# Performance work log

Measured on AMD Instinct MI355X. Metric: run time of the kernel, lower is better.

Reference implementation:

```python
import jax, jax.numpy as jnp
import numpy as np

N_NODES = 50000
N_EDGES = 800000
D_IN = 64
D_HID = 64
D_OUT = 64


def setup_inputs() -> dict:
    key = jax.random.key(0)
    ks = jax.random.split(key, 9)
    x = jax.random.normal(ks[0], (N_NODES, D_IN), dtype=jnp.float32)
    src = jax.random.randint(ks[1], (N_EDGES,), 0, N_NODES, dtype=jnp.int64)
    dst = jax.random.randint(ks[2], (N_EDGES,), 0, N_NODES, dtype=jnp.int64)
    s0 = 1.0 / np.sqrt(D_IN)
    s1 = 1.0 / np.sqrt(D_HID)
    W_self0 = jax.random.normal(ks[3], (D_IN, D_HID), dtype=jnp.float32) * s0
    W_neigh0 = jax.random.normal(ks[4], (D_IN, D_HID), dtype=jnp.float32) * s0
    b0 = jnp.zeros((D_HID,), dtype=jnp.float32)
    W_self1 = jax.random.normal(ks[5], (D_HID, D_OUT), dtype=jnp.float32) * s1
    W_neigh1 = jax.random.normal(ks[6], (D_HID, D_OUT), dtype=jnp.float32) * s1
    b1 = jnp.zeros((D_OUT,), dtype=jnp.float32)
    return {"x": x, "src": src, "dst": dst,
            "W_self0": W_self0, "W_neigh0": W_neigh0, "b0": b0,
            "W_self1": W_self1, "W_neigh1": W_neigh1, "b1": b1}


def reference(x, src, dst, W_self0, W_neigh0, b0, W_self1, W_neigh1, b1):
    n = x.shape[0]
    # in-degree per destination node; clamp to 1 for isolated nodes (DGL behavior)
    deg = jax.ops.segment_sum(jnp.ones(src.shape[0], dtype=x.dtype), dst, num_segments=n)
    inv_deg = (1.0 / jnp.maximum(deg, 1.0))[:, None]  # [N,1]

    def sage_mean(h, W_self, W_neigh, b):
        # gather src features, mean-reduce onto dst, then linear combine
        agg = jax.ops.segment_sum(h[src], dst, num_segments=n)  # [N,d]
        neigh = agg * inv_deg
        return h @ W_self + neigh @ W_neigh + b

    # layer 0: SAGEConv with internal relu activation
    h = jax.nn.relu(sage_mean(x, W_self0, W_neigh0, b0))
    # outer relu in GraphSAGE_Full.forward (idempotent after internal relu)
    h = jax.nn.relu(h)
    # dropout rate 0.0 -> identity
    # final layer: no activation
    h = sage_mean(h, W_self1, W_neigh1, b1)
    return h
```

## Files before the change

### kernel.cpp

```cpp
#include <hip/hip_runtime.h>

#define N_NODES 50000
#define N_EDGES 800000
#define D 64
#define NSLICE 8
#define SLICE_N ((N_NODES + NSLICE - 1) / NSLICE)
#define BCAP 64

__device__ __forceinline__ unsigned short f2bf(float f) {
    unsigned int u = __builtin_bit_cast(unsigned int, f);
    u += 0x7fffu + ((u >> 16) & 1u);
    return (unsigned short)(u >> 16);
}
__device__ __forceinline__ float bflo(unsigned int u) {
    return __builtin_bit_cast(float, u << 16);
}
__device__ __forceinline__ float bfhi(unsigned int u) {
    return __builtin_bit_cast(float, u & 0xffff0000u);
}

__global__ __launch_bounds__(256) void k_fill2(const int* __restrict__ src,
                                               const int* __restrict__ dst,
                                               int* __restrict__ cnt,
                                               int* __restrict__ csr) {
    int slice = blockIdx.x & (NSLICE - 1);
    int lo = slice * SLICE_N, hi = lo + SLICE_N;
    int gblk = blockIdx.x >> 3, nblk = gridDim.x >> 3;
    for (int e = gblk * blockDim.x + threadIdx.x; e < N_EDGES; e += nblk * blockDim.x) {
        int d = dst[e];
        if (d >= lo && d < hi) {
            int p = atomicAdd(&cnt[d], 1);
            csr[(d << 6) + p] = src[e];
        }
    }
}

__global__ __launch_bounds__(256, 4) void k_xform(const float* __restrict__ h,
        const float* __restrict__ Ws, const float* __restrict__ Wn,
        const float* __restrict__ b,
        float* __restrict__ yS, unsigned short* __restrict__ yN) {
    int lane = threadIdx.x & 63;
    int gwave = __builtin_amdgcn_readfirstlane((blockIdx.x * blockDim.x + threadIdx.x) >> 6);
    int nwaves = (gridDim.x * blockDim.x) >> 6;

    int mat = gwave & 1;
    const float* W = mat ? Wn : Ws;

    float w[D];
#pragma unroll
    for (int k = 0; k < D; ++k) w[k] = W[k * D + lane];
    float bj = mat ? 0.f : b[lane];

    const int ngroups = (N_NODES + 3) / 4;
    for (int g = gwave >> 1; g < ngroups; g += (nwaves >> 1)) {
        const float* x0 = h + (size_t)(g * 4) * D;
        float a0 = bj, a1 = bj, a2 = bj, a3 = bj;
#pragma unroll
        for (int kq = 0; kq < 16; ++kq) {
            float4 v0 = *(const float4*)(x0 + 0 * D + kq * 4);
            float4 v1 = *(const float4*)(x0 + 1 * D + kq * 4);
            float4 v2 = *(const float4*)(x0 + 2 * D + kq * 4);
            float4 v3 = *(const float4*)(x0 + 3 * D + kq * 4);
            a0 = fmaf(v0.x, w[kq * 4 + 0], a0);
            a1 = fmaf(v1.x, w[kq * 4 + 0], a1);
            a2 = fmaf(v2.x, w[kq * 4 + 0], a2);
            a3 = fmaf(v3.x, w[kq * 4 + 0], a3);
            a0 = fmaf(v0.y, w[kq * 4 + 1], a0);
            a1 = fmaf(v1.y, w[kq * 4 + 1], a1);
            a2 = fmaf(v2.y, w[kq * 4 + 1], a2);
            a3 = fmaf(v3.y, w[kq * 4 + 1], a3);
            a0 = fmaf(v0.z, w[kq * 4 + 2], a0);
            a1 = fmaf(v1.z, w[kq * 4 + 2], a1);
            a2 = fmaf(v2.z, w[kq * 4 + 2], a2);
            a3 = fmaf(v3.z, w[kq * 4 + 2], a3);
            a0 = fmaf(v0.w, w[kq * 4 + 3], a0);
            a1 = fmaf(v1.w, w[kq * 4 + 3], a1);
            a2 = fmaf(v2.w, w[kq * 4 + 3], a2);
            a3 = fmaf(v3.w, w[kq * 4 + 3], a3);
        }
        size_t base = (size_t)(g * 4) * D + lane;
        if (mat) {
            yN[base + 0 * D] = f2bf(a0);
            yN[base + 1 * D] = f2bf(a1);
            yN[base + 2 * D] = f2bf(a2);
            yN[base + 3 * D] = f2bf(a3);
        } else {
            yS[base + 0 * D] = a0;
            yS[base + 1 * D] = a1;
            yS[base + 2 * D] = a2;
            yS[base + 3 * D] = a3;
        }
    }
}

__global__ __launch_bounds__(256) void k_aggf(const char* __restrict__ yN,
        const float* __restrict__ yS,
        const int* __restrict__ cnt, const int* __restrict__ csr,
        float* __restrict__ out, int relu) {
    int node = __builtin_amdgcn_readfirstlane((blockIdx.x * blockDim.x + threadIdx.x) >> 6);
    int lane = threadIdx.x & 63;
    if (node >= N_NODES) return;
    int q = lane >> 4;
    int fq = lane & 15;
    int deg = cnt[node];
    const int* bucket = csr + (node << 6);
    unsigned foff = (unsigned)fq * 8u;

    float s0 = 0.f, s1 = 0.f, s2 = 0.f, s3 = 0.f;

#define ROUND16(E0)                                                         \
    {                                                                       \
        int i0 = (E0) + q, i1 = i0 + 4, i2 = i0 + 8, i3 = i0 + 12;          \
        int b0 = bucket[i0], b1 = bucket[i1], b2 = bucket[i2], b3 = bucket[i3]; \
        unsigned a0 = (i0 < deg) ? ((unsigned)b0 << 7) : 0u;                \
        unsigned a1 = (i1 < deg) ? ((unsigned)b1 << 7) : 0u;                \
        unsigned a2 = (i2 < deg) ? ((unsigned)b2 << 7) : 0u;                \
        unsigned a3 = (i3 < deg) ? ((unsigned)b3 << 7) : 0u;                \
        float m0 = (i0 < deg) ? 1.f : 0.f;                                  \
        float m1 = (i1 < deg) ? 1.f : 0.f;                                  \
        float m2 = (i2 < deg) ? 1.f : 0.f;                                  \
        float m3 = (i3 < deg) ? 1.f : 0.f;                                  \
        uint2 u0 = *(const uint2*)(yN + a0 + foff);                         \
        uint2 u1 = *(const uint2*)(yN + a1 + foff);                         \
        uint2 u2 = *(const uint2*)(yN + a2 + foff);                         \
        uint2 u3 = *(const uint2*)(yN + a3 + foff);                         \
        s0 = fmaf(m0, bflo(u0.x), s0); s0 = fmaf(m1, bflo(u1.x), s0);       \
        s0 = fmaf(m2, bflo(u2.x), s0); s0 = fmaf(m3, bflo(u3.x), s0);       \
        s1 = fmaf(m0, bfhi(u0.x), s1); s1 = fmaf(m1, bfhi(u1.x), s1);       \
        s1 = fmaf(m2, bfhi(u2.x), s1); s1 = fmaf(m3, bfhi(u3.x), s1);       \
        s2 = fmaf(m0, bflo(u0.y), s2); s2 = fmaf(m1, bflo(u1.y), s2);       \
        s2 = fmaf(m2, bflo(u2.y), s2); s2 = fmaf(m3, bflo(u3.y), s2);       \
        s3 = fmaf(m0, bfhi(u0.y), s3); s3 = fmaf(m1, bfhi(u1.y), s3);       \
        s3 = fmaf(m2, bfhi(u2.y), s3); s3 = fmaf(m3, bfhi(u3.y), s3);       \
    }

    ROUND16(0)
    if (deg > 16) ROUND16(16)
    if (deg > 32) {
        ROUND16(32)
        if (deg > 48) ROUND16(48)
    }
#undef ROUND16

    s0 += __shfl_xor(s0, 16, 64);  s0 += __shfl_xor(s0, 32, 64);
    s1 += __shfl_xor(s1, 16, 64);  s1 += __shfl_xor(s1, 32, 64);
    s2 += __shfl_xor(s2, 16, 64);  s2 += __shfl_xor(s2, 32, 64);
    s3 += __shfl_xor(s3, 16, 64);  s3 += __shfl_xor(s3, 32, 64);

    float sv = (q == 0) ? s0 : (q == 1) ? s1 : (q == 2) ? s2 : s3;
    int f = fq * 4 + q;
    float self = yS[(size_t)node * D + f];
    float inv = 1.0f / fmaxf((float)deg, 1.0f);
    float acc = self + sv * inv;
    if (relu) acc = fmaxf(acc, 0.f);
    out[(size_t)node * D + f] = acc;
}

extern "C" void kernel_launch(void* const* d_in, const int* in_sizes, int n_in,
                              void* d_out, int out_size, void* d_ws, size_t ws_size,
                              hipStream_t stream) {
    const float* x   = (const float*)d_in[0];
    const int*   src = (const int*)d_in[1];
    const int*   dst = (const int*)d_in[2];
    const float* Ws0 = (const float*)d_in[3];
    const float* Wn0 = (const float*)d_in[4];
    const float* b0  = (const float*)d_in[5];
    const float* Ws1 = (const float*)d_in[6];
    const float* Wn1 = (const float*)d_in[7];
    const float* b1  = (const float*)d_in[8];
    float* out = (float*)d_out;

    char* p = (char*)d_ws;
    float*          yS  = (float*)p;          p += (size_t)N_NODES * D * sizeof(float);
    unsigned short* yN  = (unsigned short*)p; p += (size_t)N_NODES * D * sizeof(unsigned short);
    int* cnt = (int*)p;                       p += (size_t)N_NODES * sizeof(int);
    int* csr = (int*)p;                       p += (size_t)N_NODES * BCAP * sizeof(int);

    hipMemsetAsync(cnt, 0, (size_t)N_NODES * sizeof(int), stream);

    k_fill2<<<1024, 256, 0, stream>>>(src, dst, cnt, csr);

    const int aggBlocks = (N_NODES + 3) / 4;

    k_xform<<<1024, 256, 0, stream>>>(x, Ws0, Wn0, b0, yS, yN);
    k_aggf<<<aggBlocks, 256, 0, stream>>>((const char*)yN, yS, cnt, csr, out, 1);

    k_xform<<<1024, 256, 0, stream>>>(out, Ws1, Wn1, b1, yS, yN);
    k_aggf<<<aggBlocks, 256, 0, stream>>>((const char*)yN, yS, cnt, csr, out, 0);
}
```

Before: 198.8 us.

## Split bf16 neighbor features into two half-width planes mapped to XCD halves

The transform kernel now writes the bf16 neighbor projection as two separate 32-feature arrays instead of one interleaved 64-feature array. The aggregation kernel assigns blocks so that XCDs 0-3 gather from one half-plane and XCDs 4-7 from the other. Each XCD's L2 should then only need to cache a 3.2 MB half-table rather than the full table, improving gather hit rates. Each node is now processed by two waves, each reading 64-byte rows, which doubles the bucket index reads and leaves half the lanes idle at writeback.

```diff
diff --git a/kernel.cpp b/kernel.cpp
--- a/kernel.cpp
+++ b/kernel.cpp
@@ -38,7 +38,8 @@
 __global__ __launch_bounds__(256, 4) void k_xform(const float* __restrict__ h,
         const float* __restrict__ Ws, const float* __restrict__ Wn,
         const float* __restrict__ b,
-        float* __restrict__ yS, unsigned short* __restrict__ yN) {
+        float* __restrict__ yS,
+        unsigned short* __restrict__ yNa, unsigned short* __restrict__ yNb) {
     int lane = threadIdx.x & 63;
     int gwave = __builtin_amdgcn_readfirstlane((blockIdx.x * blockDim.x + threadIdx.x) >> 6);
     int nwaves = (gridDim.x * blockDim.x) >> 6;
@@ -50,6 +51,9 @@
 #pragma unroll
     for (int k = 0; k < D; ++k) w[k] = W[k * D + lane];
     float bj = mat ? 0.f : b[lane];
+
+    unsigned short* yH = (lane < 32) ? yNa : yNb;
+    int fl = lane & 31;
 
     const int ngroups = (N_NODES + 3) / 4;
     for (int g = gwave >> 1; g < ngroups; g += (nwaves >> 1)) {
@@ -78,13 +82,14 @@
             a2 = fmaf(v2.w, w[kq * 4 + 3], a2);
             a3 = fmaf(v3.w, w[kq * 4 + 3], a3);
         }
-        size_t base = (size_t)(g * 4) * D + lane;
+        int row = g * 4;
         if (mat) {
-            yN[base + 0 * D] = f2bf(a0);
-            yN[base + 1 * D] = f2bf(a1);
-            yN[base + 2 * D] = f2bf(a2);
-            yN[base + 3 * D] = f2bf(a3);
+            yH[(row + 0) * 32 + fl] = f2bf(a0);
+            yH[(row + 1) * 32 + fl] = f2bf(a1);
+            yH[(row + 2) * 32 + fl] = f2bf(a2);
+            yH[(row + 3) * 32 + fl] = f2bf(a3);
         } else {
+            size_t base = (size_t)row * D + lane;
             yS[base + 0 * D] = a0;
             yS[base + 1 * D] = a1;
             yS[base + 2 * D] = a2;
@@ -93,37 +98,42 @@
     }
 }
 
-__global__ __launch_bounds__(256) void k_aggf(const char* __restrict__ yN,
+__global__ __launch_bounds__(256) void k_aggf2(const char* __restrict__ yA,
+        const char* __restrict__ yB,
         const float* __restrict__ yS,
         const int* __restrict__ cnt, const int* __restrict__ csr,
         float* __restrict__ out, int relu) {
-    int node = __builtin_amdgcn_readfirstlane((blockIdx.x * blockDim.x + threadIdx.x) >> 6);
+    int xcd  = blockIdx.x & 7;
+    int half = xcd >> 2;
+    int g    = (blockIdx.x >> 3) * 4 + (xcd & 3);
+    int node = __builtin_amdgcn_readfirstlane((g << 2) + (int)(threadIdx.x >> 6));
+    const char* yH = half ? yB : yA;
+    int ho = half << 5;
     int lane = threadIdx.x & 63;
-    if (node >= N_NODES) return;
-    int q = lane >> 4;
-    int fq = lane & 15;
+    int q  = lane >> 3;
+    int fq = lane & 7;
     int deg = cnt[node];
     const int* bucket = csr + (node << 6);
     unsigned foff = (unsigned)fq * 8u;
 
     float s0 = 0.f, s1 = 0.f, s2 = 0.f, s3 = 0.f;
 
-#define ROUND16(E0)                                                         \
+#define ROUND32(E0)                                                         \
     {                                                                       \
-        int i0 = (E0) + q, i1 = i0 + 4, i2 = i0 + 8, i3 = i0 + 12;          \
+        int i0 = (E0) + q, i1 = i0 + 8, i2 = i0 + 16, i3 = i0 + 24;         \
         int b0 = bucket[i0], b1 = bucket[i1], b2 = bucket[i2], b3 = bucket[i3]; \
-        unsigned a0 = (i0 < deg) ? ((unsigned)b0 << 7) : 0u;                \
-        unsigned a1 = (i1 < deg) ? ((unsigned)b1 << 7) : 0u;                \
-        unsigned a2 = (i2 < deg) ? ((unsigned)b2 << 7) : 0u;                \
-        unsigned a3 = (i3 < deg) ? ((unsigned)b3 << 7) : 0u;                \
+        unsigned a0 = (i0 < deg) ? ((unsigned)b0 << 6) : 0u;                \
+        unsigned a1 = (i1 < deg) ? ((unsigned)b1 << 6) : 0u;                \
+        unsigned a2 = (i2 < deg) ? ((unsigned)b2 << 6) : 0u;                \
+        unsigned a3 = (i3 < deg) ? ((unsigned)b3 << 6) : 0u;                \
         float m0 = (i0 < deg) ? 1.f : 0.f;                                  \
         float m1 = (i1 < deg) ? 1.f : 0.f;                                  \
         float m2 = (i2 < deg) ? 1.f : 0.f;                                  \
         float m3 = (i3 < deg) ? 1.f : 0.f;                                  \
-        uint2 u0 = *(const uint2*)(yN + a0 + foff);                         \
-        uint2 u1 = *(const uint2*)(yN + a1 + foff);                         \
-        uint2 u2 = *(const uint2*)(yN + a2 + foff);                         \
-        uint2 u3 = *(const uint2*)(yN + a3 + foff);                         \
+        uint2 u0 = *(const uint2*)(yH + a0 + foff);                         \
+        uint2 u1 = *(const uint2*)(yH + a1 + foff);                         \
+        uint2 u2 = *(const uint2*)(yH + a2 + foff);                         \
+        uint2 u3 = *(const uint2*)(yH + a3 + foff);                         \
         s0 = fmaf(m0, bflo(u0.x), s0); s0 = fmaf(m1, bflo(u1.x), s0);       \
         s0 = fmaf(m2, bflo(u2.x), s0); s0 = fmaf(m3, bflo(u3.x), s0);       \
         s1 = fmaf(m0, bfhi(u0.x), s1); s1 = fmaf(m1, bfhi(u1.x), s1);       \
@@ -134,26 +144,24 @@
         s3 = fmaf(m2, bfhi(u2.y), s3); s3 = fmaf(m3, bfhi(u3.y), s3);       \
     }
 
-    ROUND16(0)
-    if (deg > 16) ROUND16(16)
-    if (deg > 32) {
-        ROUND16(32)
-        if (deg > 48) ROUND16(48)
-    }
-#undef ROUND16
-
-    s0 += __shfl_xor(s0, 16, 64);  s0 += __shfl_xor(s0, 32, 64);
-    s1 += __shfl_xor(s1, 16, 64);  s1 += __shfl_xor(s1, 32, 64);
-    s2 += __shfl_xor(s2, 16, 64);  s2 += __shfl_xor(s2, 32, 64);
-    s3 += __shfl_xor(s3, 16, 64);  s3 += __shfl_xor(s3, 32, 64);
-
-    float sv = (q == 0) ? s0 : (q == 1) ? s1 : (q == 2) ? s2 : s3;
-    int f = fq * 4 + q;
-    float self = yS[(size_t)node * D + f];
-    float inv = 1.0f / fmaxf((float)deg, 1.0f);
-    float acc = self + sv * inv;
-    if (relu) acc = fmaxf(acc, 0.f);
-    out[(size_t)node * D + f] = acc;
+    ROUND32(0)
+    if (deg > 32) ROUND32(32)
+#undef ROUND32
+
+    s0 += __shfl_xor(s0, 8, 64); s0 += __shfl_xor(s0, 16, 64); s0 += __shfl_xor(s0, 32, 64);
+    s1 += __shfl_xor(s1, 8, 64); s1 += __shfl_xor(s1, 16, 64); s1 += __shfl_xor(s1, 32, 64);
+    s2 += __shfl_xor(s2, 8, 64); s2 += __shfl_xor(s2, 16, 64); s2 += __shfl_xor(s2, 32, 64);
+    s3 += __shfl_xor(s3, 8, 64); s3 += __shfl_xor(s3, 16, 64); s3 += __shfl_xor(s3, 32, 64);
+
+    if (q < 4) {
+        int f = ho + fq * 4 + q;
+        float self = yS[(size_t)node * D + f];
+        float inv = 1.0f / fmaxf((float)deg, 1.0f);
+        float sv = (q == 0) ? s0 : (q == 1) ? s1 : (q == 2) ? s2 : s3;
+        float acc = self + sv * inv;
+        if (relu) acc = fmaxf(acc, 0.f);
+        out[(size_t)node * D + f] = acc;
+    }
 }
 
 extern "C" void kernel_launch(void* const* d_in, const int* in_sizes, int n_in,
@@ -172,7 +180,8 @@
 
     char* p = (char*)d_ws;
     float*          yS  = (float*)p;          p += (size_t)N_NODES * D * sizeof(float);
-    unsigned short* yN  = (unsigned short*)p; p += (size_t)N_NODES * D * sizeof(unsigned short);
+    unsigned short* yNa = (unsigned short*)p; p += (size_t)N_NODES * 32 * sizeof(unsigned short);
+    unsigned short* yNb = (unsigned short*)p; p += (size_t)N_NODES * 32 * sizeof(unsigned short);
     int* cnt = (int*)p;                       p += (size_t)N_NODES * sizeof(int);
     int* csr = (int*)p;                       p += (size_t)N_NODES * BCAP * sizeof(int);
 
@@ -180,11 +189,12 @@
 
     k_fill2<<<1024, 256, 0, stream>>>(src, dst, cnt, csr);
 
-    const int aggBlocks = (N_NODES + 3) / 4;
-
-    k_xform<<<1024, 256, 0, stream>>>(x, Ws0, Wn0, b0, yS, yN);
-    k_aggf<<<aggBlocks, 256, 0, stream>>>((const char*)yN, yS, cnt, csr, out, 1);
-
-    k_xform<<<1024, 256, 0, stream>>>(out, Ws1, Wn1, b1, yS, yN);
-    k_aggf<<<aggBlocks, 256, 0, stream>>>((const char*)yN, yS, cnt, csr, out, 0);
-}
+    const int aggBlocks = 25000;
+
+    k_xform<<<1024, 256, 0, stream>>>(x, Ws0, Wn0, b0, yS, yNa, yNb);
+    k_aggf2<<<aggBlocks, 256, 0, stream>>>((const char*)yNa, (const char*)yNb,
+                                           yS, cnt, csr, out, 1);
+    k_xform<<<1024, 256, 0, stream>>>(out, Ws1, Wn1, b1, yS, yNa, yNb);
+    k_aggf2<<<aggBlocks, 256, 0, stream>>>((const char*)yNa, (const char*)yNb,
+                                           yS, cnt, csr, out, 0);
+}
```

New measurement: 211.0 us. +6.1%, slower.
